# Kernel optimization log

Measured on AMD Instinct MI355X. Metric: run time of the kernel, lower is better.

Reference implementation:

```python
import jax, jax.numpy as jnp
import numpy as np

NUM_GROUPS = 32
EPS = 1e-6
HEAD = 8


def group_norm(x, gamma, beta):
    # x: (b, c, h, w); normalize per group of channels over (c/g, h, w)
    b, c, h, w = x.shape
    g = NUM_GROUPS
    xg = x.reshape(b, g, c // g, h, w)
    mean = xg.mean(axis=(2, 3, 4), keepdims=True)
    var = xg.var(axis=(2, 3, 4), keepdims=True)
    xn = ((xg - mean) * jax.lax.rsqrt(var + EPS)).reshape(b, c, h, w)
    return xn * gamma[None, :, None, None] + beta[None, :, None, None]


def setup_inputs() -> dict:
    key = jax.random.key(0)
    ks = jax.random.split(key, 6)
    b, c, h, w = 8, 512, 64, 64
    sd = 1.0 / np.sqrt(c)
    return {
        "x": jax.random.normal(ks[0], (b, c, h, w), jnp.float32),
        "gamma": jnp.ones((c,), jnp.float32),
        "beta": jnp.zeros((c,), jnp.float32),
        "Wq": jax.random.normal(ks[1], (c, c), jnp.float32) * sd,
        "Wk": jax.random.normal(ks[2], (c, c), jnp.float32) * sd,
        "Wv": jax.random.normal(ks[3], (c, c), jnp.float32) * sd,
        "Wp": jax.random.normal(ks[4], (c, c), jnp.float32) * sd,
        "bp": jnp.zeros((c,), jnp.float32),
    }


def reference(x, gamma, beta, Wq, Wk, Wv, Wp, bp):
    b, c, h, w = x.shape
    hd = c // HEAD
    scale = jnp.sqrt(jnp.float32(hd))  # NOTE: original MULTIPLIES by sqrt(d)
    xn = group_norm(x, gamma, beta)            # (b, c, h, w)
    x_ = xn.reshape(b, c, h * w).transpose(0, 2, 1)  # (b, n, c), n = h*w
    # torch Linear: y = x @ W.T
    Q = (x_ @ Wq.T).reshape(b, h * w, HEAD, hd)
    K = (x_ @ Wk.T).reshape(b, h * w, HEAD, hd)
    V = (x_ @ Wv.T).reshape(b, h * w, HEAD, hd)
    # einsum 'bhid,bhjd->bhij' with axes (b, n, head, hd): per-position head gram
    dots = jnp.einsum('bnid,bnjd->bnij', Q, K) * scale  # (b, n, head, head)
    att = jax.nn.softmax(dots, axis=1)  # softmax over the SPATIAL axis (dim=1)
    out = jnp.einsum('bnij,bnjd->bnid', att, V).reshape(b, h * w, c)
    out = out @ Wp.T + bp  # dropout is identity at inference
    return out.transpose(0, 2, 1).reshape(b, c, h, w) + xn  # residual adds normed x
```

## Files before the change

kernel.cpp:

```cpp
#include <hip/hip_runtime.h>
#include <stdint.h>

typedef unsigned short ushort_t;
typedef _Float16 half8 __attribute__((ext_vector_type(8)));
typedef float f32x4 __attribute__((ext_vector_type(4)));

#define GLOBAL_AS __attribute__((address_space(1)))
#define LDS_AS    __attribute__((address_space(3)))

__device__ __forceinline__ float bf2f(ushort_t u) {
    union { unsigned i; float f; } v; v.i = ((unsigned)u) << 16; return v.f;
}
__device__ __forceinline__ ushort_t f2h(float f) {
    union { _Float16 h; ushort_t u; } v; v.h = (_Float16)f; return v.u;
}
__device__ __forceinline__ float h2f(ushort_t u) {
    union { _Float16 h; ushort_t u; } v; v.u = u; return (float)v.h;
}

__device__ __forceinline__ void async16(const void* g, void* l) {
    __builtin_amdgcn_global_load_lds((const GLOBAL_AS uint32_t*)g,
                                     (LDS_AS uint32_t*)l, 16, 0, 0);
}

__device__ __forceinline__ int is_bf16_in(const uint32_t* g32) {
    return *g32 == 0x3F803F80u;
}

__global__ __launch_bounds__(256) void vecconv(const void* g, const void* be, const void* bp,
                                               float* gcan, float* bcan, float* bpcan,
                                               const uint32_t* g32) {
    int t = threadIdx.x + blockIdx.x * 256;
    if (is_bf16_in(g32)) {
        gcan[t]  = bf2f(((const ushort_t*)g)[t]);
        bcan[t]  = bf2f(((const ushort_t*)be)[t]);
        bpcan[t] = bf2f(((const ushort_t*)bp)[t]);
    } else {
        gcan[t]  = ((const float*)g)[t];
        bcan[t]  = ((const float*)be)[t];
        bpcan[t] = ((const float*)bp)[t];
    }
}

__global__ __launch_bounds__(256) void wconv(const void* Wq, const void* Wk,
                                             const void* Wv, const void* Wp,
                                             ushort_t* Wh, const uint32_t* g32) {
    const void* src = (blockIdx.y == 0) ? Wq : (blockIdx.y == 1) ? Wk
                    : (blockIdx.y == 2) ? Wv : Wp;
    ushort_t* dst = Wh + (size_t)blockIdx.y * 262144;
    const int e0 = blockIdx.x * 2048 + threadIdx.x * 8;
    ushort_t o[8];
    if (is_bf16_in(g32)) {
        uint4 u = *(const uint4*)((const ushort_t*)src + e0);
        const ushort_t* e = (const ushort_t*)&u;
#pragma unroll
        for (int j = 0; j < 8; ++j) o[j] = f2h(bf2f(e[j]));
    } else {
        float4 a = *(const float4*)((const float*)src + e0);
        float4 b = *(const float4*)((const float*)src + e0 + 4);
        o[0] = f2h(a.x); o[1] = f2h(a.y); o[2] = f2h(a.z); o[3] = f2h(a.w);
        o[4] = f2h(b.x); o[5] = f2h(b.y); o[6] = f2h(b.z); o[7] = f2h(b.w);
    }
    *(uint4*)(dst + e0) = *(const uint4*)o;
}

__global__ __launch_bounds__(256) void gn_part(const void* xv, float* __restrict__ psums,
                                               const uint32_t* g32) {
    const int bx = blockIdx.x, t = threadIdx.x;
    const size_t base = (size_t)(bx >> 3) * 65536 + (size_t)(bx & 7) * 8192;
    float s = 0.f, sq = 0.f;
    if (is_bf16_in(g32)) {
        const ushort_t* p = (const ushort_t*)xv + base;
        for (int i = 0; i < 4; ++i) {
            uint4 u = ((const uint4*)p)[t + 256 * i];
            const ushort_t* e = (const ushort_t*)&u;
#pragma unroll
            for (int j = 0; j < 8; ++j) { float f = bf2f(e[j]); s += f; sq += f * f; }
        }
    } else {
        const float* p = (const float*)xv + base;
        for (int i = 0; i < 8; ++i) {
            float4 v = ((const float4*)p)[t + 256 * i];
            s += v.x + v.y + v.z + v.w;
            sq += v.x * v.x + v.y * v.y + v.z * v.z + v.w * v.w;
        }
    }
    __shared__ float ls[256], lq[256];
    ls[t] = s; lq[t] = sq;
    __syncthreads();
    for (int off = 128; off > 0; off >>= 1) {
        if (t < off) { ls[t] += ls[t + off]; lq[t] += lq[t + off]; }
        __syncthreads();
    }
    if (t == 0) { psums[bx * 2] = ls[0]; psums[bx * 2 + 1] = lq[0]; }
}

__global__ __launch_bounds__(256) void gn_fin(const float* __restrict__ psums,
                                              float* __restrict__ stats) {
    const int t = threadIdx.x;
    float s = 0.f, q = 0.f;
#pragma unroll
    for (int k = 0; k < 8; ++k) { s += psums[(t * 8 + k) * 2]; q += psums[(t * 8 + k) * 2 + 1]; }
    float mean = s * (1.f / 65536.f);
    float var  = q * (1.f / 65536.f) - mean * mean;
    stats[t * 2 + 0] = mean;
    stats[t * 2 + 1] = rsqrtf(fmaxf(var, 0.f) + 1e-6f);
}

__global__ __launch_bounds__(256) void gn_apply_t(const void* xv,
                                                  const float* __restrict__ gcan,
                                                  const float* __restrict__ bcan,
                                                  const float* __restrict__ stats,
                                                  ushort_t* __restrict__ xnt,
                                                  ushort_t* __restrict__ xnc,
                                                  const uint32_t* g32) {
    const int nt = blockIdx.x;
    const int ct = blockIdx.y;
    const int b  = blockIdx.z;
    const int t  = threadIdx.x;
    const int c0 = ct * 64, n0 = nt * 64;
    __shared__ __align__(16) ushort_t tile[64 * 80];
    if (is_bf16_in(g32)) {
        const ushort_t* x = (const ushort_t*)xv;
#pragma unroll
        for (int p = 0; p < 2; ++p) {
            int u = p * 256 + t;
            int cc = u >> 3, nc = u & 7;
            int c = c0 + cc;
            size_t gidx = ((size_t)(b * 512 + c)) * 4096 + n0 + nc * 8;
            uint4 raw = *(const uint4*)(x + gidx);
            float mean = stats[(b * 32 + (c >> 4)) * 2 + 0];
            float rstd = stats[(b * 32 + (c >> 4)) * 2 + 1];
            float sc = rstd * gcan[c];
            float sh = bcan[c] - mean * sc;
            const ushort_t* e = (const ushort_t*)&raw;
            ushort_t hv[8];
#pragma unroll
            for (int j = 0; j < 8; ++j) {
                hv[j] = f2h(bf2f(e[j]) * sc + sh);
                tile[(nc * 8 + j) * 80 + cc] = hv[j];
            }
            *(uint4*)(xnc + gidx) = *(const uint4*)hv;
        }
    } else {
        const float* x = (const float*)xv;
#pragma unroll
        for (int p = 0; p < 4; ++p) {
            int u = p * 256 + t;
            int cc = u >> 4, nc = u & 15;
            int c = c0 + cc;
            size_t gidx = ((size_t)(b * 512 + c)) * 4096 + n0 + nc * 4;
            float4 raw = *(const float4*)(x + gidx);
            float mean = stats[(b * 32 + (c >> 4)) * 2 + 0];
            float rstd = stats[(b * 32 + (c >> 4)) * 2 + 1];
            float sc = rstd * gcan[c];
            float sh = bcan[c] - mean * sc;
            ushort_t hv[4];
            hv[0] = f2h(raw.x * sc + sh);
            hv[1] = f2h(raw.y * sc + sh);
            hv[2] = f2h(raw.z * sc + sh);
            hv[3] = f2h(raw.w * sc + sh);
#pragma unroll
            for (int j = 0; j < 4; ++j) tile[(nc * 4 + j) * 80 + cc] = hv[j];
            *(uint2*)(xnc + gidx) = *(const uint2*)hv;
        }
    }
    __syncthreads();
#pragma unroll
    for (int p = 0; p < 2; ++p) {
        int u = p * 256 + t;
        int nn = u >> 3, cchunk = u & 7;
        uint4 o = *(const uint4*)(tile + nn * 80 + cchunk * 8);
        *(uint4*)(xnt + ((size_t)(b * 4096 + n0 + nn)) * 512 + c0 + cchunk * 8) = o;
    }
}

__device__ __forceinline__ void gemm128_core(const ushort_t* __restrict__ A,
                                             const ushort_t* __restrict__ B,
                                             int m0, int n0, int K, f32x4 acc[4][4]) {
    __shared__ __align__(16) ushort_t As[128 * 64];
    __shared__ __align__(16) ushort_t Bs[128 * 64];
    const int t = threadIdx.x;
    const int l = t & 63;
    const int w = t >> 6;
    const int wm = (w >> 1) * 64, wn = (w & 1) * 64;
    const int lr = l & 15, q = l >> 4;
    f32x4 zero = {0.f, 0.f, 0.f, 0.f};
#pragma unroll
    for (int mi = 0; mi < 4; ++mi)
#pragma unroll
        for (int ni = 0; ni < 4; ++ni) acc[mi][ni] = zero;

    for (int kt = 0; kt < K; kt += 64) {
        __syncthreads();
#pragma unroll
        for (int p = 0; p < 4; ++p) {
            int s = p * 256 + t;
            int r = s >> 3, c = s & 7;
            int gc = c ^ (r & 7);
            async16(A + (size_t)(m0 + r) * K + kt + gc * 8, (char*)As + p * 4096 + w * 1024);
            async16(B + (size_t)(n0 + r) * K + kt + gc * 8, (char*)Bs + p * 4096 + w * 1024);
        }
        __syncthreads();
#pragma unroll
        for (int h = 0; h < 2; ++h) {
            half8 af[4], bf[4];
#pragma unroll
            for (int mi = 0; mi < 4; ++mi) {
                int row = wm + mi * 16 + lr;
                int ch = (h * 4 + q) ^ (lr & 7);
                af[mi] = *(const half8*)(As + row * 64 + ch * 8);
            }
#pragma unroll
            for (int ni = 0; ni < 4; ++ni) {
                int row = wn + ni * 16 + lr;
                int ch = (h * 4 + q) ^ (lr & 7);
                bf[ni] = *(const half8*)(Bs + row * 64 + ch * 8);
            }
#pragma unroll
            for (int mi = 0; mi < 4; ++mi)
#pragma unroll
                for (int ni = 0; ni < 4; ++ni)
                    acc[mi][ni] = __builtin_amdgcn_mfma_f32_16x16x32_f16(af[mi], bf[ni],
                                                                        acc[mi][ni], 0, 0, 0);
        }
    }
}

__global__ __launch_bounds__(256) void gemm_qkv(const ushort_t* __restrict__ xnt,
                                                const ushort_t* __restrict__ Wh,
                                                ushort_t* __restrict__ Qo,
                                                ushort_t* __restrict__ Ko,
                                                ushort_t* __restrict__ Vo) {
    const int id = blockIdx.x;
    const int xcd = id & 7, s = id >> 3;
    const int mloc = s / 12, r = s % 12;
    const int m0 = (xcd * 32 + mloc) * 128;
    const int n0 = (r & 3) * 128;
    const int z  = r >> 2;
    const ushort_t* B = Wh + (size_t)z * 262144;
    ushort_t* C = (z == 0) ? Qo : (z == 1) ? Ko : Vo;
    f32x4 acc[4][4];
    gemm128_core(xnt, B, m0, n0, 512, acc);
    const int t = threadIdx.x, l = t & 63, w = t >> 6;
    const int wm = (w >> 1) * 64, wn = (w & 1) * 64;
    const int col = l & 15, q = l >> 4;
#pragma unroll
    for (int mi = 0; mi < 4; ++mi)
#pragma unroll
        for (int ni = 0; ni < 4; ++ni)
#pragma unroll
            for (int rr = 0; rr < 4; ++rr) {
                int row = wm + mi * 16 + q * 4 + rr;
                int cc  = wn + ni * 16 + col;
                C[(size_t)(m0 + row) * 512 + n0 + cc] = f2h(acc[mi][ni][rr]);
            }
}

__global__ __launch_bounds__(256) void dots_smax(const ushort_t* __restrict__ Q,
                                                 const ushort_t* __restrict__ K,
                                                 float* __restrict__ dots,
                                                 float* __restrict__ pmax,
                                                 float* __restrict__ psum) {
    const int chunk = blockIdx.x;
    const int t = threadIdx.x, l = t & 63, w = t >> 6;
    const int m = l & 15, q = l >> 4, col = m;
    __shared__ float sd[128][64];
    __shared__ float lm[4][64], lsum[4][64];
#pragma unroll
    for (int i = 0; i < 16; ++i) {
        int gpl = (i * 4 + w) * 2;
        int gp0 = chunk * 128 + gpl;
        const size_t base = (size_t)(gp0 + (m >> 3)) * 512 + (m & 7) * 64 + q * 8;
        half8 a0 = *(const half8*)(Q + base);
        half8 a1 = *(const half8*)(Q + base + 32);
        half8 b0 = *(const half8*)(K + base);
        half8 b1 = *(const half8*)(K + base + 32);
        f32x4 acc = {0.f, 0.f, 0.f, 0.f};
        acc = __builtin_amdgcn_mfma_f32_16x16x32_f16(a0, b0, acc, 0, 0, 0);
        acc = __builtin_amdgcn_mfma_f32_16x16x32_f16(a1, b1, acc, 0, 0, 0);
#pragma unroll
        for (int r = 0; r < 4; ++r) {
            int row = q * 4 + r;
            if (row < 8 && col < 8) {
                float v = acc[r] * 8.0f;
                int ij = row * 8 + col;
                sd[gpl][ij] = v;
                dots[(size_t)(gp0)*64 + ij] = v;
            }
            if (row >= 8 && col >= 8) {
                float v = acc[r] * 8.0f;
                int ij = (row - 8) * 8 + (col - 8);
                sd[gpl + 1][ij] = v;
                dots[(size_t)(gp0 + 1) * 64 + ij] = v;
            }
        }
    }
    __syncthreads();
    const int ij = l;
    float mx = -1e30f;
    float v[32];
#pragma unroll
    for (int r = 0; r < 32; ++r) { v[r] = sd[w * 32 + r][ij]; mx = fmaxf(mx, v[r]); }
    lm[w][ij] = mx;
    __syncthreads();
    float cm = fmaxf(fmaxf(lm[0][ij], lm[1][ij]), fmaxf(lm[2][ij], lm[3][ij]));
    float sum = 0.f;
#pragma unroll
    for (int r = 0; r < 32; ++r) sum += __expf(v[r] - cm);
    lsum[w][ij] = sum;
    __syncthreads();
    if (w == 0) {
        pmax[chunk * 64 + ij] = cm;
        psum[chunk * 64 + ij] = lsum[0][ij] + lsum[1][ij] + lsum[2][ij] + lsum[3][ij];
    }
}

__global__ __launch_bounds__(64) void smax_final(const float* __restrict__ pmax,
                                                 const float* __restrict__ psum,
                                                 float* __restrict__ Mout,
                                                 float* __restrict__ Sinv) {
    const int b = blockIdx.x;
    const int ij = threadIdx.x;
    float pm[32];
    float M = -1e30f;
#pragma unroll
    for (int c = 0; c < 32; ++c) { pm[c] = pmax[(b * 32 + c) * 64 + ij]; M = fmaxf(M, pm[c]); }
    float S = 0.f;
#pragma unroll
    for (int c = 0; c < 32; ++c) S += psum[(b * 32 + c) * 64 + ij] * __expf(pm[c] - M);
    Mout[b * 64 + ij] = M;
    Sinv[b * 64 + ij] = 1.f / S;
}

__global__ __launch_bounds__(256) void attn_apply(const float* __restrict__ dots,
                                                  const float* __restrict__ Mbuf,
                                                  const float* __restrict__ Sinv,
                                                  const ushort_t* __restrict__ V,
                                                  ushort_t* __restrict__ P) {
    const int t = threadIdx.x, l = t & 63, w = t >> 6;
    const int gp = blockIdx.x * 4 + w;
    const int b = gp >> 12;
    __shared__ float att[4][64];
    __shared__ __align__(16) ushort_t vb[4][512];
    float d = dots[(size_t)gp * 64 + l];
    att[w][l] = __expf(d - Mbuf[b * 64 + l]) * Sinv[b * 64 + l];
    *(uint4*)(&vb[w][l * 8]) = *(const uint4*)(V + (size_t)gp * 512 + l * 8);
    __syncthreads();
    const int i = l >> 3, dc = l & 7;
    float o[8] = {0, 0, 0, 0, 0, 0, 0, 0};
#pragma unroll
    for (int j = 0; j < 8; ++j) {
        float a = att[w][i * 8 + j];
        uint4 vv = *(const uint4*)(&vb[w][j * 64 + dc * 8]);
        const ushort_t* ve = (const ushort_t*)&vv;
#pragma unroll
        for (int k2 = 0; k2 < 8; ++k2) o[k2] += a * h2f(ve[k2]);
    }
    ushort_t ou[8];
#pragma unroll
    for (int k2 = 0; k2 < 8; ++k2) ou[k2] = f2h(o[k2]);
    *(uint4*)(P + (size_t)gp * 512 + l * 8) = *(const uint4*)ou;
}

__global__ __launch_bounds__(256) void gemm_out(const ushort_t* __restrict__ Wph,
                                                const ushort_t* __restrict__ P,
                                                const ushort_t* __restrict__ xnc,
                                                const float* __restrict__ bpcan,
                                                float* __restrict__ out) {
    const int id = blockIdx.x;
    const int xcd = id & 7, s = id >> 3;
    const int pair = xcd * 32 + (s >> 2);
    const int o0 = (s & 3) * 128;
    const int b  = pair >> 5;
    const int n0 = (pair & 31) * 128;
    f32x4 acc[4][4];
    gemm128_core(Wph, P + (size_t)b * 4096 * 512, o0, n0, 512, acc);
    const int t = threadIdx.x, l = t & 63, w = t >> 6;
    const int wm = (w >> 1) * 64, wn = (w & 1) * 64;
    const int col = l & 15, q = l >> 4;
#pragma unroll
    for (int mi = 0; mi < 4; ++mi) {
#pragma unroll
        for (int r = 0; r < 4; ++r) {
            int o = o0 + wm + mi * 16 + q * 4 + r;
            float bias = bpcan[o];
#pragma unroll
            for (int ni = 0; ni < 4; ++ni) {
                int n = n0 + wn + ni * 16 + col;
                size_t idx = ((size_t)(b * 512 + o)) * 4096 + n;
                out[idx] = acc[mi][ni][r] + bias + h2f(xnc[idx]);
            }
        }
    }
}

extern "C" void kernel_launch(void* const* d_in, const int* in_sizes, int n_in,
                              void* d_out, int out_size, void* d_ws, size_t ws_size,
                              hipStream_t stream) {
    const void* x     = d_in[0];
    const void* gamma = d_in[1];
    const void* beta  = d_in[2];
    const void* Wq    = d_in[3];
    const void* Wk    = d_in[4];
    const void* Wv    = d_in[5];
    const void* Wp    = d_in[6];
    const void* bp    = d_in[7];
    const uint32_t* g32 = (const uint32_t*)gamma;
    float* out = (float*)d_out;

    char* ws = (char*)d_ws;
    const size_t SZ = 33554432;
    ushort_t* xnt = (ushort_t*)(ws);
    ushort_t* Qh  = (ushort_t*)(ws + 1 * SZ);
    ushort_t* Kh  = (ushort_t*)(ws + 2 * SZ);
    ushort_t* Vh  = (ushort_t*)(ws + 3 * SZ);
    float* dots   = (float*)(ws + 4 * SZ);
    ushort_t* Wh  = (ushort_t*)(ws + 4 * SZ + 8388608);
    ushort_t* xnc = (ushort_t*)(ws + 4 * SZ + 8388608 + 2097152);
    char* tail    = ws + 4 * SZ + 8388608 + 2097152 + SZ;
    float* gcan   = (float*)(tail);
    float* bcan   = gcan + 512;
    float* bpcan  = bcan + 512;
    float* stats  = bpcan + 512;
    float* psums  = stats + 512;
    float* pmax   = psums + 4096;
    float* psumS  = pmax + 16384;
    float* Mbuf   = psumS + 16384;
    float* Sinv   = Mbuf + 512;
    ushort_t* Pb  = xnt;

    vecconv   <<<2, 256, 0, stream>>>(gamma, beta, bp, gcan, bcan, bpcan, g32);
    wconv     <<<dim3(128, 4), 256, 0, stream>>>(Wq, Wk, Wv, Wp, Wh, g32);
    gn_part   <<<2048, 256, 0, stream>>>(x, psums, g32);
    gn_fin    <<<1, 256, 0, stream>>>(psums, stats);
    gn_apply_t<<<dim3(64, 8, 8), 256, 0, stream>>>(x, gcan, bcan, stats, xnt, xnc, g32);
    gemm_qkv  <<<3072, 256, 0, stream>>>(xnt, Wh, Qh, Kh, Vh);
    dots_smax <<<256, 256, 0, stream>>>(Qh, Kh, dots, pmax, psumS);
    smax_final<<<8, 64, 0, stream>>>(pmax, psumS, Mbuf, Sinv);
    attn_apply<<<8192, 256, 0, stream>>>(dots, Mbuf, Sinv, Vh, Pb);
    gemm_out  <<<1024, 256, 0, stream>>>(Wh + 3 * 262144, Pb, xnc, bpcan, out);
}
```

Before: 292.5 us.

## Fuse tiny prep and finalize kernels into neighbors and halve GEMM K-tile

Merges the vector and weight conversion kernels into one prep launch. It folds the group-norm finalize into gn_apply_t and the softmax finalize into attn_apply, which now handles 16 positions per block. Together these remove three tiny serial launches, at the cost of each consumer block recomputing the reductions redundantly. Separately, the shared GEMM core now uses a 32-wide K tile without the XOR swizzle, so it loads less LDS per barrier but runs twice as many sync iterations and may hit more bank conflicts.

```diff
diff --git a/kernel.cpp b/kernel.cpp
--- a/kernel.cpp
+++ b/kernel.cpp
@@ -27,41 +27,43 @@
     return *g32 == 0x3F803F80u;
 }
 
-__global__ __launch_bounds__(256) void vecconv(const void* g, const void* be, const void* bp,
-                                               float* gcan, float* bcan, float* bpcan,
-                                               const uint32_t* g32) {
-    int t = threadIdx.x + blockIdx.x * 256;
-    if (is_bf16_in(g32)) {
-        gcan[t]  = bf2f(((const ushort_t*)g)[t]);
-        bcan[t]  = bf2f(((const ushort_t*)be)[t]);
-        bpcan[t] = bf2f(((const ushort_t*)bp)[t]);
+__global__ __launch_bounds__(256) void prep(const void* Wq, const void* Wk,
+                                            const void* Wv, const void* Wp,
+                                            const void* g, const void* be, const void* bp,
+                                            ushort_t* Wh, float* gcan, float* bcan,
+                                            float* bpcan, const uint32_t* g32) {
+    const int id = blockIdx.x;
+    const int isbf = is_bf16_in(g32);
+    if (id < 512) {
+        const int wsel = id >> 7, wblk = id & 127;
+        const void* src = (wsel == 0) ? Wq : (wsel == 1) ? Wk : (wsel == 2) ? Wv : Wp;
+        ushort_t* dst = Wh + (size_t)wsel * 262144;
+        const int e0 = wblk * 2048 + threadIdx.x * 8;
+        ushort_t o[8];
+        if (isbf) {
+            uint4 u = *(const uint4*)((const ushort_t*)src + e0);
+            const ushort_t* e = (const ushort_t*)&u;
+#pragma unroll
+            for (int j = 0; j < 8; ++j) o[j] = f2h(bf2f(e[j]));
+        } else {
+            float4 a = *(const float4*)((const float*)src + e0);
+            float4 b = *(const float4*)((const float*)src + e0 + 4);
+            o[0] = f2h(a.x); o[1] = f2h(a.y); o[2] = f2h(a.z); o[3] = f2h(a.w);
+            o[4] = f2h(b.x); o[5] = f2h(b.y); o[6] = f2h(b.z); o[7] = f2h(b.w);
+        }
+        *(uint4*)(dst + e0) = *(const uint4*)o;
     } else {
-        gcan[t]  = ((const float*)g)[t];
-        bcan[t]  = ((const float*)be)[t];
-        bpcan[t] = ((const float*)bp)[t];
-    }
-}
-
-__global__ __launch_bounds__(256) void wconv(const void* Wq, const void* Wk,
-                                             const void* Wv, const void* Wp,
-                                             ushort_t* Wh, const uint32_t* g32) {
-    const void* src = (blockIdx.y == 0) ? Wq : (blockIdx.y == 1) ? Wk
-                    : (blockIdx.y == 2) ? Wv : Wp;
-    ushort_t* dst = Wh + (size_t)blockIdx.y * 262144;
-    const int e0 = blockIdx.x * 2048 + threadIdx.x * 8;
-    ushort_t o[8];
-    if (is_bf16_in(g32)) {
-        uint4 u = *(const uint4*)((const ushort_t*)src + e0);
-        const ushort_t* e = (const ushort_t*)&u;
-#pragma unroll
-        for (int j = 0; j < 8; ++j) o[j] = f2h(bf2f(e[j]));
-    } else {
-        float4 a = *(const float4*)((const float*)src + e0);
-        float4 b = *(const float4*)((const float*)src + e0 + 4);
-        o[0] = f2h(a.x); o[1] = f2h(a.y); o[2] = f2h(a.z); o[3] = f2h(a.w);
-        o[4] = f2h(b.x); o[5] = f2h(b.y); o[6] = f2h(b.z); o[7] = f2h(b.w);
-    }
-    *(uint4*)(dst + e0) = *(const uint4*)o;
+        int t = threadIdx.x + (id - 512) * 256;
+        if (isbf) {
+            gcan[t]  = bf2f(((const ushort_t*)g)[t]);
+            bcan[t]  = bf2f(((const ushort_t*)be)[t]);
+            bpcan[t] = bf2f(((const ushort_t*)bp)[t]);
+        } else {
+            gcan[t]  = ((const float*)g)[t];
+            bcan[t]  = ((const float*)be)[t];
+            bpcan[t] = ((const float*)bp)[t];
+        }
+    }
 }
 
 __global__ __launch_bounds__(256) void gn_part(const void* xv, float* __restrict__ psums,
@@ -95,22 +97,10 @@
     if (t == 0) { psums[bx * 2] = ls[0]; psums[bx * 2 + 1] = lq[0]; }
 }
 
-__global__ __launch_bounds__(256) void gn_fin(const float* __restrict__ psums,
-                                              float* __restrict__ stats) {
-    const int t = threadIdx.x;
-    float s = 0.f, q = 0.f;
-#pragma unroll
-    for (int k = 0; k < 8; ++k) { s += psums[(t * 8 + k) * 2]; q += psums[(t * 8 + k) * 2 + 1]; }
-    float mean = s * (1.f / 65536.f);
-    float var  = q * (1.f / 65536.f) - mean * mean;
-    stats[t * 2 + 0] = mean;
-    stats[t * 2 + 1] = rsqrtf(fmaxf(var, 0.f) + 1e-6f);
-}
-
 __global__ __launch_bounds__(256) void gn_apply_t(const void* xv,
                                                   const float* __restrict__ gcan,
                                                   const float* __restrict__ bcan,
-                                                  const float* __restrict__ stats,
+                                                  const float* __restrict__ psums,
                                                   ushort_t* __restrict__ xnt,
                                                   ushort_t* __restrict__ xnc,
                                                   const uint32_t* g32) {
@@ -120,6 +110,24 @@
     const int t  = threadIdx.x;
     const int c0 = ct * 64, n0 = nt * 64;
     __shared__ __align__(16) ushort_t tile[64 * 80];
+    __shared__ float scS[64], shS[64];
+    if (t < 64) {
+        int c = c0 + t;
+        int g = c >> 4;
+        float s = 0.f, q = 0.f;
+#pragma unroll
+        for (int k = 0; k < 8; ++k) {
+            s += psums[((b * 32 + g) * 8 + k) * 2];
+            q += psums[((b * 32 + g) * 8 + k) * 2 + 1];
+        }
+        float mean = s * (1.f / 65536.f);
+        float var  = q * (1.f / 65536.f) - mean * mean;
+        float rstd = rsqrtf(fmaxf(var, 0.f) + 1e-6f);
+        float sc = rstd * gcan[c];
+        scS[t] = sc;
+        shS[t] = bcan[c] - mean * sc;
+    }
+    __syncthreads();
     if (is_bf16_in(g32)) {
         const ushort_t* x = (const ushort_t*)xv;
 #pragma unroll
@@ -129,10 +137,7 @@
             int c = c0 + cc;
             size_t gidx = ((size_t)(b * 512 + c)) * 4096 + n0 + nc * 8;
             uint4 raw = *(const uint4*)(x + gidx);
-            float mean = stats[(b * 32 + (c >> 4)) * 2 + 0];
-            float rstd = stats[(b * 32 + (c >> 4)) * 2 + 1];
-            float sc = rstd * gcan[c];
-            float sh = bcan[c] - mean * sc;
+            float sc = scS[cc], sh = shS[cc];
             const ushort_t* e = (const ushort_t*)&raw;
             ushort_t hv[8];
 #pragma unroll
@@ -151,10 +156,7 @@
             int c = c0 + cc;
             size_t gidx = ((size_t)(b * 512 + c)) * 4096 + n0 + nc * 4;
             float4 raw = *(const float4*)(x + gidx);
-            float mean = stats[(b * 32 + (c >> 4)) * 2 + 0];
-            float rstd = stats[(b * 32 + (c >> 4)) * 2 + 1];
-            float sc = rstd * gcan[c];
-            float sh = bcan[c] - mean * sc;
+            float sc = scS[cc], sh = shS[cc];
             ushort_t hv[4];
             hv[0] = f2h(raw.x * sc + sh);
             hv[1] = f2h(raw.y * sc + sh);
@@ -178,8 +180,8 @@
 __device__ __forceinline__ void gemm128_core(const ushort_t* __restrict__ A,
                                              const ushort_t* __restrict__ B,
                                              int m0, int n0, int K, f32x4 acc[4][4]) {
-    __shared__ __align__(16) ushort_t As[128 * 64];
-    __shared__ __align__(16) ushort_t Bs[128 * 64];
+    __shared__ __align__(16) ushort_t As[128 * 32];
+    __shared__ __align__(16) ushort_t Bs[128 * 32];
     const int t = threadIdx.x;
     const int l = t & 63;
     const int w = t >> 6;
@@ -191,39 +193,29 @@
 #pragma unroll
         for (int ni = 0; ni < 4; ++ni) acc[mi][ni] = zero;
 
-    for (int kt = 0; kt < K; kt += 64) {
+    for (int kt = 0; kt < K; kt += 32) {
         __syncthreads();
 #pragma unroll
-        for (int p = 0; p < 4; ++p) {
+        for (int p = 0; p < 2; ++p) {
             int s = p * 256 + t;
-            int r = s >> 3, c = s & 7;
-            int gc = c ^ (r & 7);
-            async16(A + (size_t)(m0 + r) * K + kt + gc * 8, (char*)As + p * 4096 + w * 1024);
-            async16(B + (size_t)(n0 + r) * K + kt + gc * 8, (char*)Bs + p * 4096 + w * 1024);
+            int r = s >> 2, kc = s & 3;
+            async16(A + (size_t)(m0 + r) * K + kt + kc * 8, (char*)As + p * 4096 + w * 1024);
+            async16(B + (size_t)(n0 + r) * K + kt + kc * 8, (char*)Bs + p * 4096 + w * 1024);
         }
         __syncthreads();
-#pragma unroll
-        for (int h = 0; h < 2; ++h) {
-            half8 af[4], bf[4];
-#pragma unroll
-            for (int mi = 0; mi < 4; ++mi) {
-                int row = wm + mi * 16 + lr;
-                int ch = (h * 4 + q) ^ (lr & 7);
-                af[mi] = *(const half8*)(As + row * 64 + ch * 8);
-            }
-#pragma unroll
-            for (int ni = 0; ni < 4; ++ni) {
-                int row = wn + ni * 16 + lr;
-                int ch = (h * 4 + q) ^ (lr & 7);
-                bf[ni] = *(const half8*)(Bs + row * 64 + ch * 8);
-            }
-#pragma unroll
-            for (int mi = 0; mi < 4; ++mi)
-#pragma unroll
-                for (int ni = 0; ni < 4; ++ni)
-                    acc[mi][ni] = __builtin_amdgcn_mfma_f32_16x16x32_f16(af[mi], bf[ni],
-                                                                        acc[mi][ni], 0, 0, 0);
-        }
+        half8 af[4], bf[4];
+#pragma unroll
+        for (int mi = 0; mi < 4; ++mi)
+            af[mi] = *(const half8*)(As + (wm + mi * 16 + lr) * 32 + q * 8);
+#pragma unroll
+        for (int ni = 0; ni < 4; ++ni)
+            bf[ni] = *(const half8*)(Bs + (wn + ni * 16 + lr) * 32 + q * 8);
+#pragma unroll
+        for (int mi = 0; mi < 4; ++mi)
+#pragma unroll
+            for (int ni = 0; ni < 4; ++ni)
+                acc[mi][ni] = __builtin_amdgcn_mfma_f32_16x16x32_f16(af[mi], bf[ni],
+                                                                    acc[mi][ni], 0, 0, 0);
     }
 }
 
@@ -316,51 +308,65 @@
     }
 }
 
-__global__ __launch_bounds__(64) void smax_final(const float* __restrict__ pmax,
-                                                 const float* __restrict__ psum,
-                                                 float* __restrict__ Mout,
-                                                 float* __restrict__ Sinv) {
-    const int b = blockIdx.x;
-    const int ij = threadIdx.x;
-    float pm[32];
-    float M = -1e30f;
-#pragma unroll
-    for (int c = 0; c < 32; ++c) { pm[c] = pmax[(b * 32 + c) * 64 + ij]; M = fmaxf(M, pm[c]); }
-    float S = 0.f;
-#pragma unroll
-    for (int c = 0; c < 32; ++c) S += psum[(b * 32 + c) * 64 + ij] * __expf(pm[c] - M);
-    Mout[b * 64 + ij] = M;
-    Sinv[b * 64 + ij] = 1.f / S;
-}
-
 __global__ __launch_bounds__(256) void attn_apply(const float* __restrict__ dots,
-                                                  const float* __restrict__ Mbuf,
-                                                  const float* __restrict__ Sinv,
+                                                  const float* __restrict__ pmax,
+                                                  const float* __restrict__ psum,
                                                   const ushort_t* __restrict__ V,
                                                   ushort_t* __restrict__ P) {
     const int t = threadIdx.x, l = t & 63, w = t >> 6;
-    const int gp = blockIdx.x * 4 + w;
-    const int b = gp >> 12;
+    const int gp_base = blockIdx.x * 16;
+    const int b = gp_base >> 12;
+    __shared__ float pm4[4][64], ps4[4][64];
+    __shared__ float Mv[64], Siv[64];
+    {
+        const int cg = w * 8;
+        float m = -1e30f;
+        float pmv[8], psv[8];
+#pragma unroll
+        for (int c = 0; c < 8; ++c) {
+            pmv[c] = pmax[(b * 32 + cg + c) * 64 + l];
+            psv[c] = psum[(b * 32 + cg + c) * 64 + l];
+            m = fmaxf(m, pmv[c]);
+        }
+        float s = 0.f;
+#pragma unroll
+        for (int c = 0; c < 8; ++c) s += psv[c] * __expf(pmv[c] - m);
+        pm4[w][l] = m; ps4[w][l] = s;
+    }
+    __syncthreads();
+    if (w == 0) {
+        float M = fmaxf(fmaxf(pm4[0][l], pm4[1][l]), fmaxf(pm4[2][l], pm4[3][l]));
+        float S = ps4[0][l] * __expf(pm4[0][l] - M) + ps4[1][l] * __expf(pm4[1][l] - M)
+                + ps4[2][l] * __expf(pm4[2][l] - M) + ps4[3][l] * __expf(pm4[3][l] - M);
+        Mv[l] = M;
+        Siv[l] = 1.f / S;
+    }
+    __syncthreads();
+    const float mv = Mv[l], siv = Siv[l];
     __shared__ float att[4][64];
     __shared__ __align__(16) ushort_t vb[4][512];
-    float d = dots[(size_t)gp * 64 + l];
-    att[w][l] = __expf(d - Mbuf[b * 64 + l]) * Sinv[b * 64 + l];
-    *(uint4*)(&vb[w][l * 8]) = *(const uint4*)(V + (size_t)gp * 512 + l * 8);
-    __syncthreads();
     const int i = l >> 3, dc = l & 7;
-    float o[8] = {0, 0, 0, 0, 0, 0, 0, 0};
-#pragma unroll
-    for (int j = 0; j < 8; ++j) {
-        float a = att[w][i * 8 + j];
-        uint4 vv = *(const uint4*)(&vb[w][j * 64 + dc * 8]);
-        const ushort_t* ve = (const ushort_t*)&vv;
-#pragma unroll
-        for (int k2 = 0; k2 < 8; ++k2) o[k2] += a * h2f(ve[k2]);
-    }
-    ushort_t ou[8];
-#pragma unroll
-    for (int k2 = 0; k2 < 8; ++k2) ou[k2] = f2h(o[k2]);
-    *(uint4*)(P + (size_t)gp * 512 + l * 8) = *(const uint4*)ou;
+    for (int p = 0; p < 4; ++p) {
+        int gp = gp_base + w * 4 + p;
+        float d = dots[(size_t)gp * 64 + l];
+        att[w][l] = __expf(d - mv) * siv;
+        *(uint4*)(&vb[w][l * 8]) = *(const uint4*)(V + (size_t)gp * 512 + l * 8);
+        __syncthreads();
+        float o[8] = {0, 0, 0, 0, 0, 0, 0, 0};
+#pragma unroll
+        for (int j = 0; j < 8; ++j) {
+            float a = att[w][i * 8 + j];
+            uint4 vv = *(const uint4*)(&vb[w][j * 64 + dc * 8]);
+            const ushort_t* ve = (const ushort_t*)&vv;
+#pragma unroll
+            for (int k2 = 0; k2 < 8; ++k2) o[k2] += a * h2f(ve[k2]);
+        }
+        ushort_t ou[8];
+#pragma unroll
+        for (int k2 = 0; k2 < 8; ++k2) ou[k2] = f2h(o[k2]);
+        *(uint4*)(P + (size_t)gp * 512 + l * 8) = *(const uint4*)ou;
+        __syncthreads();
+    }
 }
 
 __global__ __launch_bounds__(256) void gemm_out(const ushort_t* __restrict__ Wph,
@@ -422,22 +428,17 @@
     float* gcan   = (float*)(tail);
     float* bcan   = gcan + 512;
     float* bpcan  = bcan + 512;
-    float* stats  = bpcan + 512;
-    float* psums  = stats + 512;
+    float* psums  = bpcan + 512;
     float* pmax   = psums + 4096;
     float* psumS  = pmax + 16384;
-    float* Mbuf   = psumS + 16384;
-    float* Sinv   = Mbuf + 512;
     ushort_t* Pb  = xnt;
 
-    vecconv   <<<2, 256, 0, stream>>>(gamma, beta, bp, gcan, bcan, bpcan, g32);
-    wconv     <<<dim3(128, 4), 256, 0, stream>>>(Wq, Wk, Wv, Wp, Wh, g32);
+    prep      <<<514, 256, 0, stream>>>(Wq, Wk, Wv, Wp, gamma, beta, bp,
+                                        Wh, gcan, bcan, bpcan, g32);
     gn_part   <<<2048, 256, 0, stream>>>(x, psums, g32);
-    gn_fin    <<<1, 256, 0, stream>>>(psums, stats);
-    gn_apply_t<<<dim3(64, 8, 8), 256, 0, stream>>>(x, gcan, bcan, stats, xnt, xnc, g32);
+    gn_apply_t<<<dim3(64, 8, 8), 256, 0, stream>>>(x, gcan, bcan, psums, xnt, xnc, g32);
     gemm_qkv  <<<3072, 256, 0, stream>>>(xnt, Wh, Qh, Kh, Vh);
     dots_smax <<<256, 256, 0, stream>>>(Qh, Kh, dots, pmax, psumS);
-    smax_final<<<8, 64, 0, stream>>>(pmax, psumS, Mbuf, Sinv);
-    attn_apply<<<8192, 256, 0, stream>>>(dots, Mbuf, Sinv, Vh, Pb);
+    attn_apply<<<2048, 256, 0, stream>>>(dots, pmax, psumS, Vh, Pb);
     gemm_out  <<<1024, 256, 0, stream>>>(Wh + 3 * 262144, Pb, xnc, bpcan, out);
 }
```

New measurement: 287.7 us. Within noise of the previous version (-1.6%).
